# Optimization experiments

Measured on AMD Instinct MI355X. Metric: run time of the kernel, lower is better.

Reference implementation:

```python
import jax, jax.numpy as jnp
import numpy as np

B, LQ, LK = 8, 1024, 1024
DQ, DK, DV = 1024, 1024, 1024
H = 16
DEPTH = DQ // H  # 64


def setup_inputs() -> dict:
    key = jax.random.key(0)
    ks = jax.random.split(key, 6)
    query = jax.random.normal(ks[0], (B, LQ, DQ), dtype=jnp.float32)
    keys = jax.random.normal(ks[1], (B, LK, DK), dtype=jnp.float32)
    values = jax.random.normal(ks[2], (B, LK, DV), dtype=jnp.float32)
    # Per-head Linear weights (torch Linear: y = x @ W.T, W is [depth, in_dim]);
    # stacked across heads -> [H, depth, in_dim].
    Wq = jax.random.normal(ks[3], (H, DEPTH, DQ), dtype=jnp.float32) / np.sqrt(DQ).astype(np.float32)
    Wk = jax.random.normal(ks[4], (H, DEPTH, DK), dtype=jnp.float32) / np.sqrt(DK).astype(np.float32)
    Wv = jax.random.normal(ks[5], (H, DEPTH, DV), dtype=jnp.float32) / np.sqrt(DV).astype(np.float32)
    return {"query": query, "keys": keys, "values": values, "Wq": Wq, "Wk": Wk, "Wv": Wv}


def reference(query, keys, values, Wq, Wk, Wv):
    depth = Wq.shape[1]
    # Fused per-head projections (replaces the Python loop of small GEMMs)
    q = jnp.einsum('bld,hed->bhle', query, Wq)   # [B,H,Lq,depth]
    k = jnp.einsum('bsd,hed->bhse', keys, Wk)    # [B,H,Lk,depth]
    v = jnp.einsum('bsd,hed->bhse', values, Wv)  # [B,H,Lk,depth]
    scale = jnp.asarray(1.0 / np.sqrt(depth), dtype=q.dtype)
    scores = jnp.einsum('bhle,bhse->bhls', q, k) * scale  # [B,H,Lq,Lk]
    weights = jax.nn.softmax(scores, axis=-1)
    out = jnp.einsum('bhls,bhse->bhle', weights, v)       # [B,H,Lq,depth]
    bsz = query.shape[0]
    # transpose(1,2) then flatten -> [B, Lq*H*depth]
    return out.transpose(0, 2, 1, 3).reshape(bsz, -1)
```

## Files before the change

kernel.cpp:

```cpp
#include <hip/hip_runtime.h>


typedef __attribute__((ext_vector_type(8))) short short8;
typedef __attribute__((ext_vector_type(4))) float f32x4;

typedef const void __attribute__((address_space(1)))* gas_cvptr;
typedef void __attribute__((address_space(3)))* las_vptr;

__device__ __forceinline__ void gll16(const void* g, void* l) {
  __builtin_amdgcn_global_load_lds((gas_cvptr)g, (las_vptr)l, 16, 0, 0);
}

__device__ __forceinline__ unsigned short f2bf(float f) {
  unsigned u = __builtin_bit_cast(unsigned, f);
  u += 0x7fffu + ((u >> 16) & 1u);
  return (unsigned short)(u >> 16);
}

__device__ __forceinline__ unsigned pack2bf_rne(float lo, float hi) {
  return (unsigned)f2bf(lo) | ((unsigned)f2bf(hi) << 16);
}

__device__ __forceinline__ unsigned pack2bf(float a, float b) {
  unsigned ua = __builtin_bit_cast(unsigned, a) + 0x8000u;
  unsigned ub = __builtin_bit_cast(unsigned, b) + 0x8000u;
  return (ua >> 16) | (ub & 0xffff0000u);
}

__device__ __forceinline__ float fexp2(float x) {
#if __has_builtin(__builtin_amdgcn_exp2f)
  return __builtin_amdgcn_exp2f(x);
#else
  return exp2f(x);
#endif
}

#define SCALE_L2E 0.18033688011112042f
__global__ void cvt_w(const float* __restrict__ wq, const float* __restrict__ wk,
                      const float* __restrict__ wv, unsigned short* __restrict__ out) {
  long e = ((long)blockIdx.x * 256 + threadIdx.x) * 8;
  const float* src;
  float scale = 1.0f;
  if (e < 1048576) { src = wq + e; scale = SCALE_L2E; }
  else if (e < 2097152) src = wk + (e - 1048576);
  else src = wv + (e - 2097152);
  float4 a = ((const float4*)src)[0], b = ((const float4*)src)[1];
  short8 o;
  o[0] = (short)f2bf(a.x * scale); o[1] = (short)f2bf(a.y * scale);
  o[2] = (short)f2bf(a.z * scale); o[3] = (short)f2bf(a.w * scale);
  o[4] = (short)f2bf(b.x * scale); o[5] = (short)f2bf(b.y * scale);
  o[6] = (short)f2bf(b.z * scale); o[7] = (short)f2bf(b.w * scale);
  *(short8*)(out + e) = o;
}

__global__ __launch_bounds__(256, 2) void proj_gemm(
    const float* __restrict__ aq, const float* __restrict__ ak,
    const float* __restrict__ av, const unsigned short* __restrict__ bw,
    unsigned short* __restrict__ qp, unsigned short* __restrict__ kp,
    unsigned short* __restrict__ vpT) {
  __shared__ unsigned short sAB[2 * 128 * 64];
  unsigned short* sA = sAB;
  unsigned short* sB = sAB + 8192;

  const int id = blockIdx.x;
  const int xcd = id & 7, kk = id >> 3;
  const int x = kk & 7, j = kk >> 3;
  const int yz = j * 8 + xcd;
  const int z = yz >> 6, y = yz & 63;
  const float* A = z == 0 ? aq : z == 1 ? ak : av;
  const unsigned short* Bt = bw + (size_t)z * 1048576;
  unsigned short* Cp = z == 0 ? qp : z == 1 ? kp : vpT;

  const int tid = threadIdx.x;
  const int lane = tid & 63, wv = tid >> 6;
  const int quad = lane >> 4, l16 = lane & 15;
  const int wm = wv >> 1, wn = wv & 1;
  const int m0 = y * 128, n0 = x * 128;
  const int key = l16 & 7;

  f32x4 acc[4][4];
  const f32x4 zero = {0.f, 0.f, 0.f, 0.f};
#pragma unroll
  for (int i = 0; i < 4; ++i)
#pragma unroll
    for (int jj = 0; jj < 4; ++jj) acc[i][jj] = zero;

  const float* Abase = A + (size_t)m0 * 1024;

  float4 ra[4][2];
#pragma unroll
  for (int i = 0; i < 4; ++i) {
    int c = tid + i * 256;
    int row = c >> 3, cp = c & 7;
    const float* p = Abase + (size_t)row * 1024 + ((cp ^ (row & 7)) * 8);
    ra[i][0] = ((const float4*)p)[0];
    ra[i][1] = ((const float4*)p)[1];
  }

  for (int kt = 0; kt < 16; ++kt) {
    const unsigned short* Bg = Bt + (size_t)n0 * 1024 + kt * 64;
#pragma unroll
    for (int i = 0; i < 4; ++i) {
      int c = tid + i * 256;
      int row = c >> 3, cp = c & 7;
      gll16(Bg + (size_t)row * 1024 + (cp ^ (row & 7)) * 8, (char*)sB + c * 16);
    }
#pragma unroll
    for (int i = 0; i < 4; ++i) {
      int c = tid + i * 256;
      uint4 o;
      o.x = pack2bf_rne(ra[i][0].x, ra[i][0].y);
      o.y = pack2bf_rne(ra[i][0].z, ra[i][0].w);
      o.z = pack2bf_rne(ra[i][1].x, ra[i][1].y);
      o.w = pack2bf_rne(ra[i][1].z, ra[i][1].w);
      *(uint4*)((char*)sA + c * 16) = o;
    }
    __syncthreads();

    if (kt < 15) {
#pragma unroll
      for (int i = 0; i < 4; ++i) {
        int c = tid + i * 256;
        int row = c >> 3, cp = c & 7;
        const float* p = Abase + (size_t)row * 1024 + (kt + 1) * 64 +
                         ((cp ^ (row & 7)) * 8);
        ra[i][0] = ((const float4*)p)[0];
        ra[i][1] = ((const float4*)p)[1];
      }
    }

#pragma unroll
    for (int ks = 0; ks < 2; ++ks) {
      short8 af[4], bf[4];
      const int sw = ((ks * 4 + quad) ^ key) * 8;
#pragma unroll
      for (int t = 0; t < 4; ++t) {
        af[t] = *(const short8*)(sA + (wm * 64 + t * 16 + l16) * 64 + sw);
        bf[t] = *(const short8*)(sB + (wn * 64 + t * 16 + l16) * 64 + sw);
      }
#pragma unroll
      for (int mt = 0; mt < 4; ++mt)
#pragma unroll
        for (int nt = 0; nt < 4; ++nt)
          acc[mt][nt] = __builtin_amdgcn_mfma_f32_16x16x32_bf16(
              af[mt], bf[nt], acc[mt][nt], 0, 0, 0);
    }
    __syncthreads();
  }

  unsigned short* sC = sAB;
  const int h0 = x * 2;
  const int bb = m0 >> 10, l0 = m0 & 1023;
  if (z != 2) {
#pragma unroll
    for (int mt = 0; mt < 4; ++mt)
#pragma unroll
      for (int nt = 0; nt < 4; ++nt)
#pragma unroll
        for (int r = 0; r < 4; ++r)
          sC[wn * 8192 + (wm * 64 + mt * 16 + quad * 4 + r) * 64 + nt * 16 + l16] =
              f2bf(acc[mt][nt][r]);
    __syncthreads();
    const size_t base = (((size_t)(bb * 16 + h0)) * 1024 + l0) * 64;
#pragma unroll
    for (int i = 0; i < 8; ++i) {
      int ch = tid + i * 256;
      int hh = ch >> 10, inner = (ch & 1023) * 8;
      *(short8*)(Cp + base + (size_t)hh * 65536 + inner) =
          *(const short8*)(sC + hh * 8192 + inner);
    }
  } else {
#pragma unroll
    for (int mt = 0; mt < 4; ++mt)
#pragma unroll
      for (int nt = 0; nt < 4; ++nt)
#pragma unroll
        for (int r = 0; r < 4; ++r) {
          int rowIdx = wn * 64 + nt * 16 + l16;
          int l = wm * 64 + mt * 16 + quad * 4 + r;
          sC[rowIdx * 128 + (((l >> 3) ^ (rowIdx & 15)) << 3) + (l & 7)] =
              f2bf(acc[mt][nt][r]);
        }
    __syncthreads();
#pragma unroll
    for (int i = 0; i < 8; ++i) {
      int ch = tid + i * 256;
      int hh = ch >> 10, xx = ch & 1023;
      int e = xx >> 4, c = xx & 15;
      int rowIdx = hh * 64 + e;
      short8 val = *(const short8*)(sC + rowIdx * 128 + ((c ^ (rowIdx & 15)) << 3));
      *(short8*)(Cp + ((size_t)(bb * 16 + h0 + hh) << 16) + (size_t)e * 1024 + l0 + c * 8) = val;
    }
  }
}

__global__ __launch_bounds__(256, 2) void attn(
    const unsigned short* __restrict__ qp,
    const unsigned short* __restrict__ kp,
    const unsigned short* __restrict__ vpT,
    float* __restrict__ out) {
  __shared__ unsigned short sQ[256 * 64];
  __shared__ unsigned short sK[64 * 64];
  __shared__ unsigned short sV[64 * 64];
  __shared__ unsigned short sP[4][64 * 64];

  const int tid = threadIdx.x;
  const int lane = tid & 63, wv = tid >> 6;
  const int quad = lane >> 4, l16 = lane & 15;
  const int bh = blockIdx.x, qt = blockIdx.y;
  const int b = bh >> 4, h = bh & 15;
  const int key = l16 & 7;

  const unsigned short* Qg = qp + ((size_t)bh * 1024 + qt * 256) * 64;
  const unsigned short* Kg = kp + (size_t)bh * 65536;
  const unsigned short* Vg = vpT + (size_t)bh * 65536;
  unsigned short* sPw = sP[wv];

#pragma unroll
  for (int i = 0; i < 8; ++i) {
    int c = tid + i * 256;
    int row = c >> 3, cp = c & 7;
    gll16(Qg + row * 64 + (cp ^ (row & 7)) * 8, (char*)sQ + c * 16);
  }
  __syncthreads();

  short8 qfr[2][4];
#pragma unroll
  for (int ks = 0; ks < 2; ++ks) {
    const int sw = ((ks * 4 + quad) ^ key) * 8;
#pragma unroll
    for (int qc = 0; qc < 4; ++qc)
      qfr[ks][qc] = *(const short8*)(sQ + (wv * 64 + qc * 16 + l16) * 64 + sw);
  }

  const f32x4 zero = {0.f, 0.f, 0.f, 0.f};
  f32x4 oaccT[4][4];
  float lsum[4] = {0.f, 0.f, 0.f, 0.f};
#pragma unroll
  for (int et = 0; et < 4; ++et)
#pragma unroll
    for (int qc = 0; qc < 4; ++qc) oaccT[et][qc] = zero;

  for (int kt = 0; kt < 16; ++kt) {
    __syncthreads();
#pragma unroll
    for (int i = 0; i < 2; ++i) {
      int c = tid + i * 256;
      int row = c >> 3, cp = c & 7;
      gll16(Kg + (size_t)kt * 4096 + row * 64 + (cp ^ (row & 7)) * 8,
            (char*)sK + c * 16);
      gll16(Vg + (size_t)row * 1024 + kt * 64 + (cp ^ (row & 7)) * 8,
            (char*)sV + c * 16);
    }
    __syncthreads();

    f32x4 sacc[4][4];
#pragma unroll
    for (int st = 0; st < 4; ++st)
#pragma unroll
      for (int qc = 0; qc < 4; ++qc) sacc[st][qc] = zero;
#pragma unroll
    for (int ks = 0; ks < 2; ++ks) {
      short8 kfr[4];
      const int sw = ((ks * 4 + quad) ^ key) * 8;
#pragma unroll
      for (int st = 0; st < 4; ++st)
        kfr[st] = *(const short8*)(sK + (st * 16 + l16) * 64 + sw);
#pragma unroll
      for (int st = 0; st < 4; ++st)
#pragma unroll
        for (int qc = 0; qc < 4; ++qc)
          sacc[st][qc] = __builtin_amdgcn_mfma_f32_16x16x32_bf16(
              kfr[st], qfr[ks][qc], sacc[st][qc], 0, 0, 0);
    }

#pragma unroll
    for (int st = 0; st < 4; ++st)
#pragma unroll
      for (int qc = 0; qc < 4; ++qc) {
        float p0 = fexp2(sacc[st][qc][0]);
        float p1 = fexp2(sacc[st][qc][1]);
        float p2 = fexp2(sacc[st][qc][2]);
        float p3 = fexp2(sacc[st][qc][3]);
        lsum[qc] += (p0 + p1) + (p2 + p3);
        uint2 pk;
        pk.x = pack2bf(p0, p1);
        pk.y = pack2bf(p2, p3);
        int up = (st * 4 + quad) ^ (key << 1);
        *(uint2*)(sPw + (qc * 16 + l16) * 64 + up * 4) = pk;
      }

#pragma unroll
    for (int ks = 0; ks < 2; ++ks) {
      short8 vfr[4], pfr[4];
      const int sw = ((ks * 4 + quad) ^ key) * 8;
      const int swp = ((ks * 8 + quad * 2) ^ (key << 1)) * 4;
#pragma unroll
      for (int et = 0; et < 4; ++et)
        vfr[et] = *(const short8*)(sV + (et * 16 + l16) * 64 + sw);
#pragma unroll
      for (int qc = 0; qc < 4; ++qc)
        pfr[qc] = *(const short8*)(sPw + (qc * 16 + l16) * 64 + swp);
#pragma unroll
      for (int et = 0; et < 4; ++et)
#pragma unroll
        for (int qc = 0; qc < 4; ++qc)
          oaccT[et][qc] = __builtin_amdgcn_mfma_f32_16x16x32_bf16(
              vfr[et], pfr[qc], oaccT[et][qc], 0, 0, 0);
    }
  }

  float inv[4];
#pragma unroll
  for (int qc = 0; qc < 4; ++qc) {
    float l = lsum[qc];
    l += __shfl_xor(l, 16);
    l += __shfl_xor(l, 32);
    inv[qc] = 1.0f / l;
  }

#pragma unroll
  for (int et = 0; et < 4; ++et)
#pragma unroll
    for (int qc = 0; qc < 4; ++qc) {
      int qg = qt * 256 + wv * 64 + qc * 16 + l16;
      int e0 = et * 16 + quad * 4;
      float4 o;
      o.x = oaccT[et][qc][0] * inv[qc];
      o.y = oaccT[et][qc][1] * inv[qc];
      o.z = oaccT[et][qc][2] * inv[qc];
      o.w = oaccT[et][qc][3] * inv[qc];
      *(float4*)(out + ((size_t)b << 20) + (size_t)qg * 1024 + h * 64 + e0) = o;
    }
}

extern "C" void kernel_launch(void* const* d_in, const int* in_sizes, int n_in,
                              void* d_out, int out_size, void* d_ws, size_t ws_size,
                              hipStream_t stream) {
  const float* q  = (const float*)d_in[0];
  const float* k  = (const float*)d_in[1];
  const float* v  = (const float*)d_in[2];
  const float* wq = (const float*)d_in[3];
  const float* wk = (const float*)d_in[4];
  const float* wv = (const float*)d_in[5];
  float* out = (float*)d_out;

  const size_t E = (size_t)8 * 1024 * 1024;
  const size_t W = (size_t)16 * 64 * 1024;
  const size_t need = (3 * E + 3 * W) * sizeof(unsigned short);
  if (ws_size < need) return;

  unsigned short* ws  = (unsigned short*)d_ws;
  unsigned short* bw  = ws;
  unsigned short* qp  = ws + 3 * W;
  unsigned short* kp  = qp + E;
  unsigned short* vpT = qp + 2 * E;

  cvt_w<<<dim3(1536), 256, 0, stream>>>(wq, wk, wv, bw);
  proj_gemm<<<dim3(1536), 256, 0, stream>>>(q, k, v, bw, qp, kp, vpT);
  attn<<<dim3(128, 4), 256, 0, stream>>>(qp, kp, vpT, out);
}
```

Measured before the change: 263.1 us.

## Double-buffer LDS tiles in projection GEMM to overlap loads with MFMA

The projection GEMM now keeps two LDS buffers each for the A and B tiles. The next B tile is issued as an async global-to-LDS load, and the next A tile is fetched into registers, before the MFMA work on the current buffer. The bf16 conversion and store of A into the other buffer happen after the compute, and only one barrier is left per k-step. This is meant to hide global load latency behind the matrix math. In exchange it doubles the GEMM's LDS use to 64KB per block, which may limit occupancy, and it adds a sched_barrier that constrains instruction scheduling.

```diff
diff --git a/kernel.cpp b/kernel.cpp
--- a/kernel.cpp
+++ b/kernel.cpp
@@ -58,9 +58,8 @@
     const float* __restrict__ av, const unsigned short* __restrict__ bw,
     unsigned short* __restrict__ qp, unsigned short* __restrict__ kp,
     unsigned short* __restrict__ vpT) {
-  __shared__ unsigned short sAB[2 * 128 * 64];
-  unsigned short* sA = sAB;
-  unsigned short* sB = sAB + 8192;
+  __shared__ unsigned short sA[2][128 * 64];
+  __shared__ unsigned short sB[2][128 * 64];
 
   const int id = blockIdx.x;
   const int xcd = id & 7, kk = id >> 3;
@@ -86,48 +85,58 @@
     for (int jj = 0; jj < 4; ++jj) acc[i][jj] = zero;
 
   const float* Abase = A + (size_t)m0 * 1024;
-
-  float4 ra[4][2];
+  const unsigned short* Bbase = Bt + (size_t)n0 * 1024;
+
+  const int c0 = tid, c1 = tid + 256, c2 = tid + 512, c3 = tid + 768;
+  int rows[4], cols[4];
 #pragma unroll
   for (int i = 0; i < 4; ++i) {
     int c = tid + i * 256;
-    int row = c >> 3, cp = c & 7;
-    const float* p = Abase + (size_t)row * 1024 + ((cp ^ (row & 7)) * 8);
+    rows[i] = c >> 3;
+    cols[i] = ((c & 7) ^ (rows[i] & 7)) * 8;
+  }
+
+#pragma unroll
+  for (int i = 0; i < 4; ++i) {
+    int c = tid + i * 256;
+    gll16(Bbase + (size_t)rows[i] * 1024 + cols[i], (char*)sB[0] + c * 16);
+  }
+  float4 ra[4][2];
+#pragma unroll
+  for (int i = 0; i < 4; ++i) {
+    const float* p = Abase + (size_t)rows[i] * 1024 + cols[i];
     ra[i][0] = ((const float4*)p)[0];
     ra[i][1] = ((const float4*)p)[1];
   }
+#pragma unroll
+  for (int i = 0; i < 4; ++i) {
+    int c = tid + i * 256;
+    uint4 o;
+    o.x = pack2bf_rne(ra[i][0].x, ra[i][0].y);
+    o.y = pack2bf_rne(ra[i][0].z, ra[i][0].w);
+    o.z = pack2bf_rne(ra[i][1].x, ra[i][1].y);
+    o.w = pack2bf_rne(ra[i][1].z, ra[i][1].w);
+    *(uint4*)((char*)sA[0] + c * 16) = o;
+  }
+  __syncthreads();
 
   for (int kt = 0; kt < 16; ++kt) {
-    const unsigned short* Bg = Bt + (size_t)n0 * 1024 + kt * 64;
-#pragma unroll
-    for (int i = 0; i < 4; ++i) {
-      int c = tid + i * 256;
-      int row = c >> 3, cp = c & 7;
-      gll16(Bg + (size_t)row * 1024 + (cp ^ (row & 7)) * 8, (char*)sB + c * 16);
-    }
-#pragma unroll
-    for (int i = 0; i < 4; ++i) {
-      int c = tid + i * 256;
-      uint4 o;
-      o.x = pack2bf_rne(ra[i][0].x, ra[i][0].y);
-      o.y = pack2bf_rne(ra[i][0].z, ra[i][0].w);
-      o.z = pack2bf_rne(ra[i][1].x, ra[i][1].y);
-      o.w = pack2bf_rne(ra[i][1].z, ra[i][1].w);
-      *(uint4*)((char*)sA + c * 16) = o;
-    }
-    __syncthreads();
-
+    const int cur = kt & 1, nxt = cur ^ 1;
     if (kt < 15) {
 #pragma unroll
       for (int i = 0; i < 4; ++i) {
         int c = tid + i * 256;
-        int row = c >> 3, cp = c & 7;
-        const float* p = Abase + (size_t)row * 1024 + (kt + 1) * 64 +
-                         ((cp ^ (row & 7)) * 8);
+        gll16(Bbase + (size_t)rows[i] * 1024 + (kt + 1) * 64 + cols[i],
+              (char*)sB[nxt] + c * 16);
+      }
+#pragma unroll
+      for (int i = 0; i < 4; ++i) {
+        const float* p = Abase + (size_t)rows[i] * 1024 + (kt + 1) * 64 + cols[i];
         ra[i][0] = ((const float4*)p)[0];
         ra[i][1] = ((const float4*)p)[1];
       }
     }
+    __builtin_amdgcn_sched_barrier(0);
 
 #pragma unroll
     for (int ks = 0; ks < 2; ++ks) {
@@ -135,8 +144,8 @@
       const int sw = ((ks * 4 + quad) ^ key) * 8;
 #pragma unroll
       for (int t = 0; t < 4; ++t) {
-        af[t] = *(const short8*)(sA + (wm * 64 + t * 16 + l16) * 64 + sw);
-        bf[t] = *(const short8*)(sB + (wn * 64 + t * 16 + l16) * 64 + sw);
+        af[t] = *(const short8*)(sA[cur] + (wm * 64 + t * 16 + l16) * 64 + sw);
+        bf[t] = *(const short8*)(sB[cur] + (wn * 64 + t * 16 + l16) * 64 + sw);
       }
 #pragma unroll
       for (int mt = 0; mt < 4; ++mt)
@@ -145,10 +154,23 @@
           acc[mt][nt] = __builtin_amdgcn_mfma_f32_16x16x32_bf16(
               af[mt], bf[nt], acc[mt][nt], 0, 0, 0);
     }
-    __syncthreads();
-  }
-
-  unsigned short* sC = sAB;
+
+    if (kt < 15) {
+#pragma unroll
+      for (int i = 0; i < 4; ++i) {
+        int c = tid + i * 256;
+        uint4 o;
+        o.x = pack2bf_rne(ra[i][0].x, ra[i][0].y);
+        o.y = pack2bf_rne(ra[i][0].z, ra[i][0].w);
+        o.z = pack2bf_rne(ra[i][1].x, ra[i][1].y);
+        o.w = pack2bf_rne(ra[i][1].z, ra[i][1].w);
+        *(uint4*)((char*)sA[nxt] + c * 16) = o;
+      }
+    }
+    __syncthreads();
+  }
+
+  unsigned short* sC = &sA[0][0];
   const int h0 = x * 2;
   const int bb = m0 >> 10, l0 = m0 & 1023;
   if (z != 2) {
```

Result: slower. 285.1 us (+8.3%).
